# Kernel optimization log

Measured on AMD Instinct MI355X. Metric: run time of the kernel, lower is better.

Reference implementation:

```python
import jax, jax.numpy as jnp
import numpy as np

B, Q, C, H, D, E, I = 8, 256, 192, 20, 64, 1500, 5120
HID = H * D  # 1280
EPS = 1e-5
SCALE = D ** -0.5


def _linear(x, w, b):
    return jnp.einsum('bsh,oh->bso', x, w) + b


def _layernorm(x, w, b):
    xf = x.astype(jnp.float32)
    mu = jnp.mean(xf, axis=-1, keepdims=True)
    var = jnp.mean(jnp.square(xf - mu), axis=-1, keepdims=True)
    return ((xf - mu) * jax.lax.rsqrt(var + EPS) * w + b).astype(x.dtype)


def _heads(x):  # [B,S,HID] -> [B,H,S,D]
    return x.reshape(B, -1, H, D).transpose(0, 2, 1, 3)


def setup_inputs() -> dict:
    key = jax.random.key(0)
    ks = jax.random.split(key, 24)
    s = 0.02
    inp = {
        'hidden_states': jax.random.normal(ks[0], (B, Q, HID), jnp.float32),
        'mask': jnp.zeros((B, 1, Q, Q + C), jnp.float32),
        'past_key': jax.random.normal(ks[1], (B, H, C, D), jnp.float32),
        'past_value': jax.random.normal(ks[2], (B, H, C, D), jnp.float32),
        'cross_key': jax.random.normal(ks[3], (B, H, E, D), jnp.float32),
        'cross_value': jax.random.normal(ks[4], (B, H, E, D), jnp.float32),
        'q_w': jax.random.normal(ks[5], (HID, HID), jnp.float32) * s,
        'q_b': jnp.zeros((HID,), jnp.float32),
        'k_w': jax.random.normal(ks[6], (HID, HID), jnp.float32) * s,
        'k_b': jnp.zeros((HID,), jnp.float32),
        'v_w': jax.random.normal(ks[7], (HID, HID), jnp.float32) * s,
        'v_b': jnp.zeros((HID,), jnp.float32),
        'o_w': jax.random.normal(ks[8], (HID, HID), jnp.float32) * s,
        'o_b': jnp.zeros((HID,), jnp.float32),
        'cq_w': jax.random.normal(ks[9], (HID, HID), jnp.float32) * s,
        'cq_b': jnp.zeros((HID,), jnp.float32),
        'co_w': jax.random.normal(ks[10], (HID, HID), jnp.float32) * s,
        'co_b': jnp.zeros((HID,), jnp.float32),
        'up_w': jax.random.normal(ks[11], (I, HID), jnp.float32) * s,
        'up_b': jnp.zeros((I,), jnp.float32),
        'down_w': jax.random.normal(ks[12], (HID, I), jnp.float32) * s,
        'down_b': jnp.zeros((HID,), jnp.float32),
        'ln1_w': jnp.ones((HID,), jnp.float32),
        'ln1_b': jnp.zeros((HID,), jnp.float32),
        'ln2_w': jnp.ones((HID,), jnp.float32),
        'ln2_b': jnp.zeros((HID,), jnp.float32),
        'ln3_w': jnp.ones((HID,), jnp.float32),
        'ln3_b': jnp.zeros((HID,), jnp.float32),
    }
    return inp


def reference(hidden_states, mask, past_key, past_value, cross_key, cross_value,
              q_w, q_b, k_w, k_b, v_w, v_b, o_w, o_b,
              cq_w, cq_b, co_w, co_b, up_w, up_b, down_w, down_b,
              ln1_w, ln1_b, ln2_w, ln2_b, ln3_w, ln3_b):
    # ---- self-attention block ----
    residual = hidden_states
    x = _layernorm(hidden_states, ln1_w, ln1_b)
    q = _heads(_linear(x, q_w, q_b) * SCALE)          # [B,H,Q,D]
    k_new = _heads(_linear(x, k_w, k_b))              # [B,H,Q,D]
    v_new = _heads(_linear(x, v_w, v_b))
    k = jnp.concatenate([past_key, k_new], axis=2)    # [B,H,C+Q,D]
    v = jnp.concatenate([past_value, v_new], axis=2)
    scores = jnp.einsum('bhqd,bhkd->bhqk', q, k) + mask
    attn = jnp.einsum('bhqk,bhkd->bhqd', jax.nn.softmax(scores, axis=-1), v)
    attn = attn.transpose(0, 2, 1, 3).reshape(B, Q, HID)
    attn_out = _linear(attn, o_w, o_b)
    present_key = k[:, :, Q:, :]
    present_value = v[:, :, Q:, :]
    h = residual + attn_out
    # ---- cross-attention block ----
    residual = h
    x = _layernorm(h, ln2_w, ln2_b)
    cq = _heads(_linear(x, cq_w, cq_b) * SCALE)       # [B,H,Q,D]
    cscores = jnp.einsum('bhqd,bhkd->bhqk', cq, cross_key)
    cattn = jnp.einsum('bhqk,bhkd->bhqd', jax.nn.softmax(cscores, axis=-1), cross_value)
    cattn = cattn.transpose(0, 2, 1, 3).reshape(B, Q, HID)
    h = residual + _linear(cattn, co_w, co_b)
    # ---- MLP block ----
    residual = h
    x = _layernorm(h, ln3_w, ln3_b)
    up = _linear(x, up_w, up_b)
    mlp_out = _linear(jax.nn.gelu(up, approximate=False), down_w, down_b)
    h = residual + mlp_out
    return (h, present_key, present_value)
```

## Files before the change

### kernel.cpp

```cpp
#include <hip/hip_runtime.h>
#include <math.h>

#define Bc   8
#define Qn   256
#define Cn   192
#define Hn   20
#define Dn   64
#define En   1500
#define In   5120
#define HIDn 1280
#define BQ   2048
#define KSELF 448
#define S1   (BQ*HIDn)
#define WSZ  (HIDn*HIDn)

typedef __attribute__((ext_vector_type(8))) short bf16x8;
typedef __attribute__((ext_vector_type(4))) float f32x4;

__device__ __forceinline__ short f2bf(float f) {
  union { float f; unsigned u; } x; x.f = f;
  unsigned r = x.u + 0x7fffu + ((x.u >> 16) & 1u);
  return (short)(r >> 16);
}
__device__ __forceinline__ float bf2f(short s) {
  union { unsigned u; float f; } x; x.u = ((unsigned)(unsigned short)s) << 16;
  return x.f;
}
__device__ __forceinline__ void gload16(const short* g, short* l) {
  __builtin_amdgcn_global_load_lds(
      (const __attribute__((address_space(1))) void*)g,
      (__attribute__((address_space(3))) void*)l, 16, 0, 0);
}

__global__ __launch_bounds__(256) void convert_all(
    const float* q, const float* k, const float* v, const float* o,
    const float* cq, const float* co, const float* up, const float* dn,
    short* wq, short* wk, short* wv, short* wo,
    short* wcq, short* wco, short* wup, short* wdn)
{
  const float* src; short* dst; int n;
  switch (blockIdx.y) {
    case 0: src = q;  dst = wq;  n = WSZ; break;
    case 1: src = k;  dst = wk;  n = WSZ; break;
    case 2: src = v;  dst = wv;  n = WSZ; break;
    case 3: src = o;  dst = wo;  n = WSZ; break;
    case 4: src = cq; dst = wcq; n = WSZ; break;
    case 5: src = co; dst = wco; n = WSZ; break;
    case 6: src = up; dst = wup; n = HIDn * In; break;
    default: src = dn; dst = wdn; n = HIDn * In; break;
  }
  const int i = (blockIdx.x * 256 + threadIdx.x) * 8;
  if (i >= n) return;
  const float4 a = *reinterpret_cast<const float4*>(src + i);
  const float4 b = *reinterpret_cast<const float4*>(src + i + 4);
  bf16x8 t;
  t[0] = f2bf(a.x); t[1] = f2bf(a.y); t[2] = f2bf(a.z); t[3] = f2bf(a.w);
  t[4] = f2bf(b.x); t[5] = f2bf(b.y); t[6] = f2bf(b.z); t[7] = f2bf(b.w);
  *reinterpret_cast<bf16x8*>(dst + i) = t;
}

__global__ __launch_bounds__(256) void layernorm_k(
    const float* __restrict__ in, const float* __restrict__ w,
    const float* __restrict__ b, short* __restrict__ out)
{
  const int row = blockIdx.x;
  const float* x = in + (size_t)row * HIDn;
  float v[5], s = 0.f, s2 = 0.f;
#pragma unroll
  for (int i = 0; i < 5; ++i) {
    float t = x[threadIdx.x + 256 * i];
    v[i] = t; s += t; s2 += t * t;
  }
#pragma unroll
  for (int off = 1; off < 64; off <<= 1) {
    s  += __shfl_xor(s,  off, 64);
    s2 += __shfl_xor(s2, off, 64);
  }
  __shared__ float red[8];
  const int wave = threadIdx.x >> 6, lane = threadIdx.x & 63;
  if (lane == 0) { red[wave] = s; red[wave + 4] = s2; }
  __syncthreads();
  s  = red[0] + red[1] + red[2] + red[3];
  s2 = red[4] + red[5] + red[6] + red[7];
  const float mu  = s / HIDn;
  const float var = s2 / HIDn - mu * mu;
  const float rs  = rsqrtf(var + 1e-5f);
#pragma unroll
  for (int i = 0; i < 5; ++i) {
    const int c = threadIdx.x + 256 * i;
    out[(size_t)row * HIDn + c] = f2bf((v[i] - mu) * rs * w[c] + b[c]);
  }
}

template<int BM, int BN, int MODE>
__global__ __launch_bounds__(256) void gemm_bk64(
    const short* __restrict__ A, const short* __restrict__ W,
    const float* __restrict__ bias, const float* __restrict__ resid,
    void* __restrict__ out0, void* __restrict__ out1, void* __restrict__ out2,
    const float* __restrict__ b1, const float* __restrict__ b2,
    int N, int K, float scale)
{
  constexpr int FM = BM / 32, FN = BN / 32;
  __shared__ __align__(16) short Alds[BM * 64];
  __shared__ __align__(16) short Blds[BN * 64];
  const int tid = threadIdx.x, lane = tid & 63, wave = tid >> 6;
  const int wr = wave >> 1, wc = wave & 1;
  const int m0 = blockIdx.x * BM, n0 = blockIdx.y * BN;
  const int lr = lane & 15;
  const int kc = (lane >> 4) * 8;

  f32x4 acc[FM][FN];
#pragma unroll
  for (int mi = 0; mi < FM; ++mi)
#pragma unroll
    for (int ni = 0; ni < FN; ++ni)
      acc[mi][ni] = (f32x4){0.f, 0.f, 0.f, 0.f};

  const int nk = K >> 6;
  for (int kt = 0; kt < nk; ++kt) {
    const int k0 = kt << 6;
#pragma unroll
    for (int j = 0; j < BM / 32; ++j) {
      const int i = wave + 4 * j;
      const int rb = i >> 1, kk = i & 1;
      gload16(A + (size_t)(m0 + rb * 16 + lr) * K + k0 + kk * 32 + kc, &Alds[i * 512]);
    }
#pragma unroll
    for (int j = 0; j < BN / 32; ++j) {
      const int i = wave + 4 * j;
      const int rb = i >> 1, kk = i & 1;
      gload16(W + (size_t)(n0 + rb * 16 + lr) * K + k0 + kk * 32 + kc, &Blds[i * 512]);
    }
    __syncthreads();
    bf16x8 af[2][FM], bfv[2][FN];
#pragma unroll
    for (int kk = 0; kk < 2; ++kk) {
#pragma unroll
      for (int mi = 0; mi < FM; ++mi)
        af[kk][mi] = *reinterpret_cast<const bf16x8*>(
            &Alds[((wr * FM + mi) * 2 + kk) * 512 + lane * 8]);
#pragma unroll
      for (int ni = 0; ni < FN; ++ni)
        bfv[kk][ni] = *reinterpret_cast<const bf16x8*>(
            &Blds[((wc * FN + ni) * 2 + kk) * 512 + lane * 8]);
    }
#pragma unroll
    for (int kk = 0; kk < 2; ++kk)
#pragma unroll
      for (int mi = 0; mi < FM; ++mi)
#pragma unroll
        for (int ni = 0; ni < FN; ++ni)
          acc[mi][ni] = __builtin_amdgcn_mfma_f32_16x16x32_bf16(
              af[kk][mi], bfv[kk][ni], acc[mi][ni], 0, 0, 0);
    __syncthreads();
  }

  const int cn = lane & 15;
  const int rb = (lane >> 4) * 4;
#pragma unroll
  for (int mi = 0; mi < FM; ++mi)
#pragma unroll
    for (int ni = 0; ni < FN; ++ni)
#pragma unroll
      for (int j = 0; j < 4; ++j) {
        const int row = m0 + wr * (BM / 2) + mi * 16 + rb + j;
        const int col = n0 + wc * (BN / 2) + ni * 16 + cn;
        const float a = acc[mi][ni][j];
        if (MODE == 0) {
          ((float*)out0)[(size_t)row * N + col] =
              a + bias[col] + resid[(size_t)row * N + col];
        } else if (MODE == 1) {
          ((short*)out0)[(size_t)row * N + col] = f2bf((a + bias[col]) * scale);
        } else if (MODE == 2) {
          float t = a + bias[col];
          t = 0.5f * t * (1.f + erff(t * 0.70710678118654752f));
          ((short*)out0)[(size_t)row * N + col] = f2bf(t);
        } else {
          const int rg  = n0 / 1280;
          const int cl  = col - rg * 1280;
          short* op     = rg == 0 ? (short*)out0 : rg == 1 ? (short*)out1 : (short*)out2;
          const float* bp = rg == 0 ? bias : rg == 1 ? b1 : b2;
          const float sc  = rg == 0 ? 0.125f : 1.f;
          op[(size_t)row * 1280 + cl] = f2bf((a + bp[cl]) * sc);
        }
      }
}

template<bool HASMASK>
__global__ __launch_bounds__(256) void attn_mfma(
    const short* __restrict__ Qb, const float* __restrict__ Kp,
    const float* __restrict__ Vp, const short* __restrict__ Kn,
    const short* __restrict__ Vn, const float* __restrict__ mask,
    short* __restrict__ Ob, int Cp, int KT)
{
  const int orig = blockIdx.x;
  const int idx  = (orig & 7) * 80 + (orig >> 3);
  const int qt = idx & 3;
  const int h  = (idx >> 2) % Hn;
  const int b  = idx / (4 * Hn);
  const int tid = threadIdx.x, lane = tid & 63, wave = tid >> 6;
  const int q0 = qt * 64;
  const int cn = lane & 15;
  const int hg = lane >> 4;
  const int rb = hg * 4;

  __shared__ __align__(16) short k_s[64][72];
  __shared__ __align__(16) short vt_s[64][72];
  __shared__ __align__(16) short p_s[4][16][72];

  bf16x8 aq[2];
  {
    const short* qrow = Qb + (size_t)(b * Qn + q0 + wave * 16 + cn) * HIDn + h * 64;
    aq[0] = *reinterpret_cast<const bf16x8*>(qrow + hg * 8);
    aq[1] = *reinterpret_cast<const bf16x8*>(qrow + 32 + hg * 8);
  }

  float mrun[4] = {-1e30f, -1e30f, -1e30f, -1e30f};
  float lrun[4] = {0.f, 0.f, 0.f, 0.f};
  f32x4 oacc[4];
#pragma unroll
  for (int t = 0; t < 4; ++t) oacc[t] = (f32x4){0.f, 0.f, 0.f, 0.f};

  const int nchunk = (KT + 63) >> 6;
  for (int ci = 0; ci < nchunk; ++ci) {
    const int c0 = ci * 64;
    for (int i = tid; i < 64 * 8; i += 256) {
      const int key = i >> 3, d8 = (i & 7) * 8;
      const int gk = c0 + key;
      bf16x8 kv8 = (bf16x8)0, vv8 = (bf16x8)0;
      if (gk < KT) {
        if (gk < Cp) {
          const size_t off = (((size_t)b * Hn + h) * (size_t)Cp + gk) * 64 + d8;
          const float4 ka = *reinterpret_cast<const float4*>(Kp + off);
          const float4 kb = *reinterpret_cast<const float4*>(Kp + off + 4);
          const float4 va = *reinterpret_cast<const float4*>(Vp + off);
          const float4 vb = *reinterpret_cast<const float4*>(Vp + off + 4);
          kv8[0] = f2bf(ka.x); kv8[1] = f2bf(ka.y); kv8[2] = f2bf(ka.z); kv8[3] = f2bf(ka.w);
          kv8[4] = f2bf(kb.x); kv8[5] = f2bf(kb.y); kv8[6] = f2bf(kb.z); kv8[7] = f2bf(kb.w);
          vv8[0] = f2bf(va.x); vv8[1] = f2bf(va.y); vv8[2] = f2bf(va.z); vv8[3] = f2bf(va.w);
          vv8[4] = f2bf(vb.x); vv8[5] = f2bf(vb.y); vv8[6] = f2bf(vb.z); vv8[7] = f2bf(vb.w);
        } else {
          const size_t off = (size_t)(b * Qn + (gk - Cp)) * HIDn + h * 64 + d8;
          kv8 = *reinterpret_cast<const bf16x8*>(Kn + off);
          vv8 = *reinterpret_cast<const bf16x8*>(Vn + off);
        }
      }
      *reinterpret_cast<bf16x8*>(&k_s[key][d8]) = kv8;
      const int g = key >> 3, o = key & 7, f = (d8 >> 3) & 7;
#pragma unroll
      for (int j = 0; j < 8; ++j)
        vt_s[d8 + j][((g ^ f) << 3) | o] = vv8[j];
    }
    __syncthreads();

    f32x4 sacc[4];
#pragma unroll
    for (int t = 0; t < 4; ++t) sacc[t] = (f32x4){0.f, 0.f, 0.f, 0.f};
#pragma unroll
    for (int t = 0; t < 4; ++t)
#pragma unroll
      for (int kk = 0; kk < 2; ++kk) {
        const bf16x8 bk = *reinterpret_cast<const bf16x8*>(&k_s[t * 16 + cn][kk * 32 + hg * 8]);
        sacc[t] = __builtin_amdgcn_mfma_f32_16x16x32_bf16(aq[kk], bk, sacc[t], 0, 0, 0);
      }

    float sc[4][4];
#pragma unroll
    for (int t = 0; t < 4; ++t) {
      const int key = c0 + t * 16 + cn;
      const bool valid = key < KT;
#pragma unroll
      for (int j = 0; j < 4; ++j) {
        float v = sacc[t][j];
        if (HASMASK && valid)
          v += mask[((size_t)(b * Qn) + q0 + wave * 16 + rb + j) * KT + key];
        sc[t][j] = valid ? v : -1e30f;
      }
    }

#pragma unroll
    for (int j = 0; j < 4; ++j) {
      float mx = fmaxf(fmaxf(sc[0][j], sc[1][j]), fmaxf(sc[2][j], sc[3][j]));
#pragma unroll
      for (int off = 1; off < 16; off <<= 1) mx = fmaxf(mx, __shfl_xor(mx, off, 64));
      const float mnew  = fmaxf(mrun[j], mx);
      const float alpha = __expf(mrun[j] - mnew);
      float ps = 0.f;
#pragma unroll
      for (int t = 0; t < 4; ++t) {
        const float p = __expf(sc[t][j] - mnew);
        sc[t][j] = p; ps += p;
      }
#pragma unroll
      for (int off = 1; off < 16; off <<= 1) ps += __shfl_xor(ps, off, 64);
      lrun[j] = lrun[j] * alpha + ps;
      mrun[j] = mnew;
#pragma unroll
      for (int t = 0; t < 4; ++t) oacc[t][j] *= alpha;
    }

#pragma unroll
    for (int t = 0; t < 4; ++t)
#pragma unroll
      for (int j = 0; j < 4; ++j)
        p_s[wave][rb + j][t * 16 + cn] = f2bf(sc[t][j]);

    const bf16x8 ap0 = *reinterpret_cast<const bf16x8*>(&p_s[wave][cn][hg * 8]);
    const bf16x8 ap1 = *reinterpret_cast<const bf16x8*>(&p_s[wave][cn][32 + hg * 8]);
#pragma unroll
    for (int t = 0; t < 4; ++t) {
      const int d  = t * 16 + cn;
      const int fd = (d >> 3) & 7;
      const bf16x8 bv0 = *reinterpret_cast<const bf16x8*>(&vt_s[d][((hg)     ^ fd) << 3]);
      const bf16x8 bv1 = *reinterpret_cast<const bf16x8*>(&vt_s[d][((4 + hg) ^ fd) << 3]);
      oacc[t] = __builtin_amdgcn_mfma_f32_16x16x32_bf16(ap0, bv0, oacc[t], 0, 0, 0);
      oacc[t] = __builtin_amdgcn_mfma_f32_16x16x32_bf16(ap1, bv1, oacc[t], 0, 0, 0);
    }
    __syncthreads();
  }

#pragma unroll
  for (int t = 0; t < 4; ++t)
#pragma unroll
    for (int j = 0; j < 4; ++j)
      Ob[(size_t)(b * Qn + q0 + wave * 16 + rb + j) * HIDn + h * 64 + t * 16 + cn] =
          f2bf(oacc[t][j] / lrun[j]);
}

__global__ __launch_bounds__(256) void copy_present(
    const short* __restrict__ kn, const short* __restrict__ vn,
    float* __restrict__ outk, float* __restrict__ outv)
{
  const int idx = blockIdx.x * 256 + threadIdx.x;
  if (idx >= Bc * Hn * Cn * 8) return;
  const int d8 = (idx & 7) * 8;
  int t = idx >> 3;
  const int c = t % Cn; t /= Cn;
  const int h = t % Hn;
  const int b = t / Hn;
  const size_t src = (size_t)(b * Qn + (Qn - Cn) + c) * HIDn + h * 64 + d8;
  const size_t dst = (((size_t)b * Hn + h) * Cn + c) * 64 + d8;
  const bf16x8 kv = *reinterpret_cast<const bf16x8*>(kn + src);
  const bf16x8 vv = *reinterpret_cast<const bf16x8*>(vn + src);
#pragma unroll
  for (int j = 0; j < 8; ++j) {
    outk[dst + j] = bf2f(kv[j]);
    outv[dst + j] = bf2f(vv[j]);
  }
}

extern "C" void kernel_launch(void* const* d_in, const int* in_sizes, int n_in,
                              void* d_out, int out_size, void* d_ws, size_t ws_size,
                              hipStream_t stream)
{
  const float* hidden  = (const float*)d_in[0];
  const float* mask    = (const float*)d_in[1];
  const float* past_k  = (const float*)d_in[2];
  const float* past_v  = (const float*)d_in[3];
  const float* cross_k = (const float*)d_in[4];
  const float* cross_v = (const float*)d_in[5];
  const float* q_w  = (const float*)d_in[6];  const float* q_b  = (const float*)d_in[7];
  const float* k_w  = (const float*)d_in[8];  const float* k_b  = (const float*)d_in[9];
  const float* v_w  = (const float*)d_in[10]; const float* v_b  = (const float*)d_in[11];
  const float* o_w  = (const float*)d_in[12]; const float* o_b  = (const float*)d_in[13];
  const float* cq_w = (const float*)d_in[14]; const float* cq_b = (const float*)d_in[15];
  const float* co_w = (const float*)d_in[16]; const float* co_b = (const float*)d_in[17];
  const float* up_w = (const float*)d_in[18]; const float* up_b = (const float*)d_in[19];
  const float* dn_w = (const float*)d_in[20]; const float* dn_b = (const float*)d_in[21];
  const float* ln1w = (const float*)d_in[22]; const float* ln1b = (const float*)d_in[23];
  const float* ln2w = (const float*)d_in[24]; const float* ln2b = (const float*)d_in[25];
  const float* ln3w = (const float*)d_in[26]; const float* ln3b = (const float*)d_in[27];

  short* wq  = (short*)d_ws;
  short* wk  = wq  + (size_t)WSZ;
  short* wv  = wk  + (size_t)WSZ;
  short* wo  = wv  + (size_t)WSZ;
  short* wcq = wo  + (size_t)WSZ;
  short* wco = wcq + (size_t)WSZ;
  short* wup = wco + (size_t)WSZ;
  short* wdn = wup + (size_t)HIDn * In;
  short* xb  = wdn + (size_t)HIDn * In;
  short* qb  = xb  + (size_t)S1;
  short* kb  = qb  + (size_t)S1;
  short* vb  = kb  + (size_t)S1;
  short* ab  = vb  + (size_t)S1;
  short* upa = ab  + (size_t)S1;
  float* h1  = (float*)(upa + (size_t)BQ * In);
  float* h2  = h1 + (size_t)S1;

  float* out_h  = (float*)d_out;
  float* out_pk = out_h + (size_t)S1;
  float* out_pv = out_pk + (size_t)(Bc * Hn * Cn * Dn);

  const dim3 blk(256);
  const dim3 gconv(3200, 8);
  const dim3 gqkv(16, 30);
  const dim3 gn64(16, 20);
  const dim3 gup(16, 40);
  const dim3 gattn(640);

  convert_all<<<gconv, blk, 0, stream>>>(q_w, k_w, v_w, o_w, cq_w, co_w, up_w, dn_w,
                                         wq, wk, wv, wo, wcq, wco, wup, wdn);
  layernorm_k<<<BQ, blk, 0, stream>>>(hidden, ln1w, ln1b, xb);
  gemm_bk64<128, 128, 3><<<gqkv, blk, 0, stream>>>(xb, wq, q_b, nullptr,
      qb, kb, vb, k_b, v_b, 3840, HIDn, 1.f);
  copy_present<<<(Bc * Hn * Cn * 8 + 255) / 256, blk, 0, stream>>>(kb, vb, out_pk, out_pv);
  attn_mfma<true><<<gattn, blk, 0, stream>>>(qb, past_k, past_v, kb, vb, mask, ab, Cn, KSELF);
  gemm_bk64<128, 64, 0><<<gn64, blk, 0, stream>>>(ab, wo, o_b, hidden,
      h1, nullptr, nullptr, nullptr, nullptr, HIDn, HIDn, 1.f);
  layernorm_k<<<BQ, blk, 0, stream>>>(h1, ln2w, ln2b, xb);
  gemm_bk64<128, 64, 1><<<gn64, blk, 0, stream>>>(xb, wcq, cq_b, nullptr,
      qb, nullptr, nullptr, nullptr, nullptr, HIDn, HIDn, 0.125f);
  attn_mfma<false><<<gattn, blk, 0, stream>>>(qb, cross_k, cross_v,
      (const short*)nullptr, (const short*)nullptr, nullptr, ab, En, En);
  gemm_bk64<128, 64, 0><<<gn64, blk, 0, stream>>>(ab, wco, co_b, h1,
      h2, nullptr, nullptr, nullptr, nullptr, HIDn, HIDn, 1.f);
  layernorm_k<<<BQ, blk, 0, stream>>>(h2, ln3w, ln3b, xb);
  gemm_bk64<128, 128, 2><<<gup, blk, 0, stream>>>(xb, wup, up_b, nullptr,
      upa, nullptr, nullptr, nullptr, nullptr, In, HIDn, 1.f);
  gemm_bk64<128, 64, 0><<<gn64, blk, 0, stream>>>(upa, wdn, dn_b, h2,
      out_h, nullptr, nullptr, nullptr, nullptr, HIDn, In, 1.f);
}
```

Before: 521.5 us.

## Halve GEMM M-tiles, add XCD-aware block remap, split-K down projection

Every GEMM now uses 64-row tiles, which doubles the number of workgroups and gives better coverage of the many CUs. A block-index remap interleaves workgroups across the 8 XCDs so neighbouring tiles share L2. The K=5120 down projection is split into two halves whose fp32 partials go into dead scratch buffers, and a new elementwise kernel sums them with bias and residual. The trade-off is less data reuse per tile, plus an extra launch and extra fp32 traffic for the reduction.

```diff
diff --git a/kernel.cpp b/kernel.cpp
--- a/kernel.cpp
+++ b/kernel.cpp
@@ -98,16 +98,26 @@
     const float* __restrict__ bias, const float* __restrict__ resid,
     void* __restrict__ out0, void* __restrict__ out1, void* __restrict__ out2,
     const float* __restrict__ b1, const float* __restrict__ b2,
-    int N, int K, float scale)
+    int N, int K, int LDK, float scale)
 {
   constexpr int FM = BM / 32, FN = BN / 32;
   __shared__ __align__(16) short Alds[BM * 64];
   __shared__ __align__(16) short Blds[BN * 64];
+
+  const int GX = gridDim.x, GY = gridDim.y;
+  int lid = blockIdx.x + GX * (blockIdx.y + GY * blockIdx.z);
+  const int cpx = (GX * GY * gridDim.z) >> 3;
+  lid = (lid & 7) * cpx + (lid >> 3);
+  const int bx = lid % GX;
+  const int by = (lid / GX) % GY;
+  const int bz = lid / (GX * GY);
+
   const int tid = threadIdx.x, lane = tid & 63, wave = tid >> 6;
   const int wr = wave >> 1, wc = wave & 1;
-  const int m0 = blockIdx.x * BM, n0 = blockIdx.y * BN;
+  const int m0 = bx * BM, n0 = by * BN;
   const int lr = lane & 15;
   const int kc = (lane >> 4) * 8;
+  const size_t koff = (size_t)bz * K;
 
   f32x4 acc[FM][FN];
 #pragma unroll
@@ -123,13 +133,15 @@
     for (int j = 0; j < BM / 32; ++j) {
       const int i = wave + 4 * j;
       const int rb = i >> 1, kk = i & 1;
-      gload16(A + (size_t)(m0 + rb * 16 + lr) * K + k0 + kk * 32 + kc, &Alds[i * 512]);
+      gload16(A + (size_t)(m0 + rb * 16 + lr) * LDK + koff + k0 + kk * 32 + kc,
+              &Alds[i * 512]);
     }
 #pragma unroll
     for (int j = 0; j < BN / 32; ++j) {
       const int i = wave + 4 * j;
       const int rb = i >> 1, kk = i & 1;
-      gload16(W + (size_t)(n0 + rb * 16 + lr) * K + k0 + kk * 32 + kc, &Blds[i * 512]);
+      gload16(W + (size_t)(n0 + rb * 16 + lr) * LDK + koff + k0 + kk * 32 + kc,
+              &Blds[i * 512]);
     }
     __syncthreads();
     bf16x8 af[2][FM], bfv[2][FN];
@@ -175,15 +187,38 @@
           float t = a + bias[col];
           t = 0.5f * t * (1.f + erff(t * 0.70710678118654752f));
           ((short*)out0)[(size_t)row * N + col] = f2bf(t);
-        } else {
+        } else if (MODE == 3) {
           const int rg  = n0 / 1280;
           const int cl  = col - rg * 1280;
           short* op     = rg == 0 ? (short*)out0 : rg == 1 ? (short*)out1 : (short*)out2;
           const float* bp = rg == 0 ? bias : rg == 1 ? b1 : b2;
           const float sc  = rg == 0 ? 0.125f : 1.f;
           op[(size_t)row * 1280 + cl] = f2bf((a + bp[cl]) * sc);
+        } else {
+          float* op = bz == 0 ? (float*)out0 : (float*)out1;
+          op[(size_t)row * N + col] = a;
         }
       }
+}
+
+__global__ __launch_bounds__(256) void reduce_down(
+    const float* __restrict__ p0, const float* __restrict__ p1,
+    const float* __restrict__ resid, const float* __restrict__ bias,
+    float* __restrict__ out)
+{
+  const size_t i = ((size_t)blockIdx.x * 256 + threadIdx.x) * 4;
+  if (i >= (size_t)S1) return;
+  const int col = (int)(i % HIDn);
+  const float4 a = *reinterpret_cast<const float4*>(p0 + i);
+  const float4 b = *reinterpret_cast<const float4*>(p1 + i);
+  const float4 r = *reinterpret_cast<const float4*>(resid + i);
+  const float4 bi = *reinterpret_cast<const float4*>(bias + col);
+  float4 o;
+  o.x = a.x + b.x + r.x + bi.x;
+  o.y = a.y + b.y + r.y + bi.y;
+  o.z = a.z + b.z + r.z + bi.z;
+  o.w = a.w + b.w + r.w + bi.w;
+  *reinterpret_cast<float4*>(out + i) = o;
 }
 
 template<bool HASMASK>
@@ -387,6 +422,8 @@
   short* upa = ab  + (size_t)S1;
   float* h1  = (float*)(upa + (size_t)BQ * In);
   float* h2  = h1 + (size_t)S1;
+  float* p0  = (float*)qb;
+  float* p1  = (float*)vb;
 
   float* out_h  = (float*)d_out;
   float* out_pk = out_h + (size_t)S1;
@@ -394,30 +431,32 @@
 
   const dim3 blk(256);
   const dim3 gconv(3200, 8);
-  const dim3 gqkv(16, 30);
-  const dim3 gn64(16, 20);
-  const dim3 gup(16, 40);
+  const dim3 gqkv(32, 30);
+  const dim3 g64(32, 20);
+  const dim3 gup(32, 40);
+  const dim3 gdn(32, 20, 2);
   const dim3 gattn(640);
 
   convert_all<<<gconv, blk, 0, stream>>>(q_w, k_w, v_w, o_w, cq_w, co_w, up_w, dn_w,
                                          wq, wk, wv, wo, wcq, wco, wup, wdn);
   layernorm_k<<<BQ, blk, 0, stream>>>(hidden, ln1w, ln1b, xb);
-  gemm_bk64<128, 128, 3><<<gqkv, blk, 0, stream>>>(xb, wq, q_b, nullptr,
-      qb, kb, vb, k_b, v_b, 3840, HIDn, 1.f);
+  gemm_bk64<64, 128, 3><<<gqkv, blk, 0, stream>>>(xb, wq, q_b, nullptr,
+      qb, kb, vb, k_b, v_b, 3840, HIDn, HIDn, 1.f);
   copy_present<<<(Bc * Hn * Cn * 8 + 255) / 256, blk, 0, stream>>>(kb, vb, out_pk, out_pv);
   attn_mfma<true><<<gattn, blk, 0, stream>>>(qb, past_k, past_v, kb, vb, mask, ab, Cn, KSELF);
-  gemm_bk64<128, 64, 0><<<gn64, blk, 0, stream>>>(ab, wo, o_b, hidden,
-      h1, nullptr, nullptr, nullptr, nullptr, HIDn, HIDn, 1.f);
+  gemm_bk64<64, 64, 0><<<g64, blk, 0, stream>>>(ab, wo, o_b, hidden,
+      h1, nullptr, nullptr, nullptr, nullptr, HIDn, HIDn, HIDn, 1.f);
   layernorm_k<<<BQ, blk, 0, stream>>>(h1, ln2w, ln2b, xb);
-  gemm_bk64<128, 64, 1><<<gn64, blk, 0, stream>>>(xb, wcq, cq_b, nullptr,
-      qb, nullptr, nullptr, nullptr, nullptr, HIDn, HIDn, 0.125f);
+  gemm_bk64<64, 64, 1><<<g64, blk, 0, stream>>>(xb, wcq, cq_b, nullptr,
+      qb, nullptr, nullptr, nullptr, nullptr, HIDn, HIDn, HIDn, 0.125f);
   attn_mfma<false><<<gattn, blk, 0, stream>>>(qb, cross_k, cross_v,
       (const short*)nullptr, (const short*)nullptr, nullptr, ab, En, En);
-  gemm_bk64<128, 64, 0><<<gn64, blk, 0, stream>>>(ab, wco, co_b, h1,
-      h2, nullptr, nullptr, nullptr, nullptr, HIDn, HIDn, 1.f);
+  gemm_bk64<64, 64, 0><<<g64, blk, 0, stream>>>(ab, wco, co_b, h1,
+      h2, nullptr, nullptr, nullptr, nullptr, HIDn, HIDn, HIDn, 1.f);
   layernorm_k<<<BQ, blk, 0, stream>>>(h2, ln3w, ln3b, xb);
-  gemm_bk64<128, 128, 2><<<gup, blk, 0, stream>>>(xb, wup, up_b, nullptr,
-      upa, nullptr, nullptr, nullptr, nullptr, In, HIDn, 1.f);
-  gemm_bk64<128, 64, 0><<<gn64, blk, 0, stream>>>(upa, wdn, dn_b, h2,
-      out_h, nullptr, nullptr, nullptr, nullptr, HIDn, In, 1.f);
-}
+  gemm_bk64<64, 128, 2><<<gup, blk, 0, stream>>>(xb, wup, up_b, nullptr,
+      upa, nullptr, nullptr, nullptr, nullptr, In, HIDn, HIDn, 1.f);
+  gemm_bk64<64, 64, 4><<<gdn, blk, 0, stream>>>(upa, wdn, nullptr, nullptr,
+      p0, p1, nullptr, nullptr, nullptr, HIDn, In / 2, In, 1.f);
+  reduce_down<<<(S1 / 4 + 255) / 256, blk, 0, stream>>>(p0, p1, h2, dn_b, out_h);
+}
```

Measured after the change: 541.7 us. 3.9% more time.
